# Performance work log

Hardware: AMD Instinct MI355X
Metric: run time of the kernel (lower is better)

The kernel has to match this reference:

```python
import jax, jax.numpy as jnp
import numpy as np

N, T, J, NB = 2048, 81, 16, 15
D_ATT, HEADS, SEQ, D_LIN, NOISE = 48, 6, 31, 256, 45
BN_EPS, LN_EPS, SLOPE = 1e-5, 1e-6, 0.01

# Human3.6M 16-joint skeleton bone (parent, child) pairs
_BONES = [(0,1),(1,2),(2,3),(0,4),(4,5),(5,6),(0,7),(7,8),(8,9),(9,10),(8,11),(11,12),(12,13),(8,14),(14,15)]
BONES_P = np.array([p for p, c in _BONES])
BONES_C = np.array([c for p, c in _BONES])
_parent = {c: p for p, c in _BONES}
_bone_of = {c: i for i, (p, c) in enumerate(_BONES)}
_M = np.zeros((NB, J), np.float32)  # M[i,j]=1 iff bone i lies on root->joint j chain
for j in range(1, J):
    jj = j
    while jj != 0:
        _M[_bone_of[jj], j] = 1.0
        jj = _parent[jj]
M_BONE2POSE = jnp.asarray(_M)
FIXED_MASK = jnp.ones((NB,), jnp.float32).at[jnp.array([6, 7])].set(0.0)  # torso bones kept fixed


def _layer_norm(t, a, b):
    mean = t.mean(-1, keepdims=True)
    # torch.std default is unbiased (ddof=1); module divides by (std + eps)
    std = jnp.sqrt(((t - mean) ** 2).sum(-1, keepdims=True) / (t.shape[-1] - 1))
    return a * (t - mean) / (std + LN_EPS) + b


def _leaky(x):
    return jnp.where(x >= 0, x, SLOPE * x)


def _axis_angle_to_matrix(v):
    # Rodrigues: v (..., 3) axis-angle -> (..., 3, 3)
    theta = jnp.linalg.norm(v, axis=-1, keepdims=True)
    k = v / jnp.maximum(theta, 1e-8)
    c = jnp.cos(theta)[..., None]
    s = jnp.sin(theta)[..., None]
    kx, ky, kz = k[..., 0], k[..., 1], k[..., 2]
    z = jnp.zeros_like(kx)
    K = jnp.stack([jnp.stack([z, -kz, ky], -1),
                   jnp.stack([kz, z, -kx], -1),
                   jnp.stack([-ky, kx, z], -1)], -2)
    kk = k[..., :, None] * k[..., None, :]
    return c * jnp.eye(3, dtype=v.dtype) + s * K + (1 - c) * kk


def setup_inputs() -> dict:
    key = jax.random.key(0)
    ks = jax.random.split(key, 12)
    w = lambda k, shape, scale=0.05: jax.random.normal(k, shape, jnp.float32) * scale
    return {
        'inputs_3d': jax.random.normal(ks[0], (N, 1, T, J, 3), jnp.float32),
        'noise': jax.random.normal(ks[1], (N, NOISE), jnp.float32),
        'enc_w': w(ks[2], (D_ATT, 3)), 'enc_b': jnp.zeros((D_ATT,), jnp.float32),
        'enc_bn_g': jnp.ones((D_ATT,), jnp.float32), 'enc_bn_b': jnp.zeros((D_ATT,), jnp.float32),
        'ln_a': jnp.ones((D_ATT,), jnp.float32), 'ln_b': jnp.zeros((D_ATT,), jnp.float32),
        'wq': w(ks[3], (D_ATT, D_ATT)), 'bq': jnp.zeros((D_ATT,), jnp.float32),
        'wk': w(ks[4], (D_ATT, D_ATT)), 'bk': jnp.zeros((D_ATT,), jnp.float32),
        'wv': w(ks[5], (D_ATT, D_ATT)), 'bv': jnp.zeros((D_ATT,), jnp.float32),
        'wo': w(ks[6], (D_ATT, D_ATT)), 'bo': jnp.zeros((D_ATT,), jnp.float32),
        'w1': w(ks[7], (D_LIN, SEQ * D_ATT)), 'b1': jnp.zeros((D_LIN,), jnp.float32),
        'bn1_g': jnp.ones((D_LIN,), jnp.float32), 'bn1_b': jnp.zeros((D_LIN,), jnp.float32),
        'w2': w(ks[8], (NB * 4, D_LIN)), 'b2': w(ks[9], (NB * 4,), 0.1),
    }


def reference(inputs_3d, noise, enc_w, enc_b, enc_bn_g, enc_bn_b, ln_a, ln_b,
              wq, bq, wk, bk, wv, bv, wo, bo, w1, b1, bn1_g, bn1_b, w2, b2):
    x5 = inputs_3d[:, 0]                                  # (n, T, 16, 3)
    root = x5[:, :, :1, :]
    x = x5 - root                                         # root-centered
    bvec = x[..., BONES_C, :] - x[..., BONES_P, :]        # (n, T, 15, 3)
    blen = jnp.linalg.norm(bvec, axis=-1, keepdims=True)
    bunit = bvec / blen
    n, t_len = x.shape[0], x.shape[1]
    mid = (t_len - 1) // 2

    x_ = x[:, mid].reshape(n, -1)                         # (n, 48)
    y = jnp.concatenate([x_, noise], axis=-1).reshape(n, SEQ, 3)
    # Conv1d(k=1) == per-token linear; BatchNorm eval (running mean 0, var 1); Dropout off
    y = jax.nn.relu((y @ enc_w.T + enc_b) * enc_bn_g / jnp.sqrt(1.0 + BN_EPS) + enc_bn_b)

    # tiny 6-head self-attention with pre-LayerNorm and residual
    h = _layer_norm(y, ln_a, ln_b)
    d = D_ATT // HEADS
    q = (h @ wq.T + bq).reshape(n, SEQ, HEADS, d).transpose(0, 2, 1, 3)
    k = (h @ wk.T + bk).reshape(n, SEQ, HEADS, d).transpose(0, 2, 1, 3)
    v = (h @ wv.T + bv).reshape(n, SEQ, HEADS, d).transpose(0, 2, 1, 3)
    probs = jax.nn.softmax(jnp.einsum('nhqd,nhkd->nhqk', q, k) / (d ** 0.5), axis=-1)
    ctx = jnp.einsum('nhqk,nhkd->nhqd', probs, v).transpose(0, 2, 1, 3).reshape(n, SEQ, D_ATT)
    y = y + (ctx @ wo.T + bo)

    y = y.reshape(n, -1)                                  # (n, 1488)
    y = _leaky((y @ w1.T + b1) * bn1_g / jnp.sqrt(1.0 + BN_EPS) + bn1_b)
    y = _leaky(y @ w2.T + b2).reshape(n, NB, 4)           # (n, 15, 4)

    axis = y[..., :3]
    axis = axis / jnp.linalg.norm(axis, axis=-1, keepdims=True)
    theta = y[..., 3:4] / t_len                           # (n, 15, 1)
    t_idx = jnp.arange(t_len, dtype=y.dtype)              # (T,)
    vaa = axis[:, None] * (theta[:, None] * t_idx[None, :, None, None])  # (n, T, 15, 3)
    R = _axis_angle_to_matrix(vaa)                        # (n, T, 15, 3, 3)
    mod_unit = jnp.einsum('ntbij,ntbj->ntbi', R, bunit)
    mask = FIXED_MASK[None, None, :, None]
    mod_unit = mod_unit * mask + bunit * (1 - mask)
    ba_diff = 1 - jnp.sum(mod_unit * bunit, axis=-1)      # (n, T, 15)
    mod_bone = mod_unit * blen
    out = jnp.einsum('ntbc,bj->ntjc', mod_bone, M_BONE2POSE) + root  # (n, T, 16, 3)
    return out, ba_diff
```

## Files before the change

kernel.cpp:

```cpp
#include <hip/hip_runtime.h>
#include <math.h>

#define NS   2048
#define TL   81
#define NBN  15
#define DA   48
#define SQL  31
#define KD   1488
#define DL   256
#define MID  40

#define INV_SQRT_BN 0.99999500003749969f
#define SCALE_ATT   0.35355339059327373f

__global__ __launch_bounds__(256)
void attn_kernel(const float* __restrict__ x5, const float* __restrict__ noise,
                 const float* __restrict__ enc_w, const float* __restrict__ enc_b,
                 const float* __restrict__ enc_g, const float* __restrict__ enc_bb,
                 const float* __restrict__ ln_a, const float* __restrict__ ln_b,
                 const float* __restrict__ wq, const float* __restrict__ bq,
                 const float* __restrict__ wk, const float* __restrict__ bk,
                 const float* __restrict__ wv, const float* __restrict__ bv,
                 const float* __restrict__ wo, const float* __restrict__ bo,
                 float* __restrict__ y2)
{
    __shared__ float s93[96];
    __shared__ float sy[32*49];
    __shared__ float sh[32*49];
    __shared__ float sW[3*48*49];
    __shared__ __align__(16) float sQKV[32*148];
    __shared__ float smean[32], sinv[32];

    const int tid = threadIdx.x;
    const int n = blockIdx.x;

    if (tid < 93) {
        float v;
        if (tid < 48) {
            const float* base = x5 + ((size_t)n*TL + MID)*48;
            v = base[tid] - base[tid % 3];
        } else {
            v = noise[(size_t)n*45 + (tid-48)];
        }
        s93[tid] = v;
    }
    #pragma unroll
    for (int l=0; l<9; l++){
        int idx = tid + l*256;
        int f = idx/48, c = idx - f*48;
        int o = f*49 + c;
        sW[o]        = wq[idx];
        sW[2352 + o] = wk[idx];
        sW[4704 + o] = wv[idx];
    }
    __syncthreads();

    for (int idx=tid; idx<SQL*DA; idx+=256){
        int s = idx/48, f = idx - s*48;
        float a = enc_b[f]
                + s93[s*3+0]*enc_w[f*3+0]
                + s93[s*3+1]*enc_w[f*3+1]
                + s93[s*3+2]*enc_w[f*3+2];
        float v = a * (enc_g[f]*INV_SQRT_BN) + enc_bb[f];
        sy[s*49+f] = fmaxf(v, 0.0f);
    }
    __syncthreads();

    if (tid < SQL){
        float m = 0.f;
        for (int f=0; f<48; f++) m += sy[tid*49+f];
        m *= (1.0f/48.0f);
        float vs = 0.f;
        for (int f=0; f<48; f++){ float d = sy[tid*49+f]-m; vs += d*d; }
        float sd = sqrtf(vs * (1.0f/47.0f));
        smean[tid] = m;
        sinv[tid]  = 1.0f/(sd + 1e-6f);
    }
    __syncthreads();

    for (int idx=tid; idx<SQL*DA; idx+=256){
        int s = idx/48, f = idx - s*48;
        sh[s*49+f] = ln_a[f]*(sy[s*49+f]-smean[s])*sinv[s] + ln_b[f];
    }
    __syncthreads();

    if (tid < 192){
        const int sg = tid/24, fg = tid - (tid/24)*24;
        const int arr = fg >> 3;
        const int f0  = (fg & 7)*6;
        const float* wb = sW + arr*2352 + f0*49;
        const float* hb = sh + sg*4*49;
        float a0[6]={0,0,0,0,0,0}, a1[6]={0,0,0,0,0,0};
        float a2[6]={0,0,0,0,0,0}, a3[6]={0,0,0,0,0,0};
        for (int c=0; c<48; c++){
            float h0 = hb[c], h1 = hb[49+c], h2 = hb[98+c], h3 = hb[147+c];
            #pragma unroll
            for (int i=0;i<6;i++){
                float w = wb[i*49+c];
                a0[i] += h0*w; a1[i] += h1*w; a2[i] += h2*w; a3[i] += h3*w;
            }
        }
        const float* bias = (arr==0)? bq : (arr==1? bk : bv);
        #pragma unroll
        for (int i=0;i<6;i++){
            float b = bias[f0+i];
            int col = arr*48 + f0 + i;
            sQKV[(sg*4+0)*148 + col] = a0[i] + b;
            sQKV[(sg*4+1)*148 + col] = a1[i] + b;
            sQKV[(sg*4+2)*148 + col] = a2[i] + b;
            sQKV[(sg*4+3)*148 + col] = a3[i] + b;
        }
    }
    __syncthreads();

    #pragma unroll
    for (int l=0; l<9; l++){
        int idx = tid + l*256;
        sW[(idx/48)*49 + (idx%48)] = wo[idx];
    }
    if (tid < 186){
        const int hd = tid/31, qi = tid - (tid/31)*31;
        const float4 q0 = *(const float4*)(sQKV + qi*148 + hd*8);
        const float4 q1 = *(const float4*)(sQKV + qi*148 + hd*8 + 4);
        float sc[31]; float mx = -1e30f;
        for (int ki=0; ki<31; ki++){
            const float4 k0 = *(const float4*)(sQKV + ki*148 + 48 + hd*8);
            const float4 k1 = *(const float4*)(sQKV + ki*148 + 48 + hd*8 + 4);
            float d = q0.x*k0.x + q0.y*k0.y + q0.z*k0.z + q0.w*k0.w
                    + q1.x*k1.x + q1.y*k1.y + q1.z*k1.z + q1.w*k1.w;
            d *= SCALE_ATT;
            sc[ki] = d; mx = fmaxf(mx, d);
        }
        float ssum = 0.f;
        for (int ki=0; ki<31; ki++){ float e = expf(sc[ki]-mx); sc[ki]=e; ssum += e; }
        float rin = 1.0f/ssum;
        float4 c0 = {0,0,0,0}, c1 = {0,0,0,0};
        for (int ki=0; ki<31; ki++){
            float p = sc[ki];
            const float4 v0 = *(const float4*)(sQKV + ki*148 + 96 + hd*8);
            const float4 v1 = *(const float4*)(sQKV + ki*148 + 96 + hd*8 + 4);
            c0.x += p*v0.x; c0.y += p*v0.y; c0.z += p*v0.z; c0.w += p*v0.w;
            c1.x += p*v1.x; c1.y += p*v1.y; c1.z += p*v1.z; c1.w += p*v1.w;
        }
        float* cb = sh + qi*49 + hd*8;
        cb[0]=c0.x*rin; cb[1]=c0.y*rin; cb[2]=c0.z*rin; cb[3]=c0.w*rin;
        cb[4]=c1.x*rin; cb[5]=c1.y*rin; cb[6]=c1.z*rin; cb[7]=c1.w*rin;
    }
    __syncthreads();

    if (tid < 192){
        const int sg = tid/12, fg = tid - (tid/12)*12;
        const int f0 = fg*4;
        const float* wb = sW + f0*49;
        const float* cb = sh + sg*2*49;
        float a0[4]={0,0,0,0}, a1[4]={0,0,0,0};
        for (int c=0; c<48; c++){
            float x0 = cb[c], x1 = cb[49+c];
            #pragma unroll
            for (int i=0;i<4;i++){
                float w = wb[i*49+c];
                a0[i] += x0*w; a1[i] += x1*w;
            }
        }
        {
            int s = sg*2;
            if (s < 31){
                float* dst = y2 + (size_t)n*KD + s*48 + f0;
                const float* yb = sy + s*49 + f0;
                #pragma unroll
                for (int i=0;i<4;i++) dst[i] = yb[i] + a0[i] + bo[f0+i];
            }
        }
        {
            int s = sg*2+1;
            if (s < 31){
                float* dst = y2 + (size_t)n*KD + s*48 + f0;
                const float* yb = sy + s*49 + f0;
                #pragma unroll
                for (int i=0;i<4;i++) dst[i] = yb[i] + a1[i] + bo[f0+i];
            }
        }
    }
}

#define KSP 6
#define KPS 248
#define KCH 8

__global__ __launch_bounds__(256)
void gemm1_kernel(const float* __restrict__ y2, const float* __restrict__ w1,
                  float* __restrict__ y3raw, int use_partial)
{
    __shared__ __align__(16) float sB[KCH*256];
    __shared__ __align__(16) float sA[KCH*20];
    const int tid = threadIdx.x;
    const int bx = blockIdx.x;
    const int m0 = (bx & 127) * 16;
    const int split = bx >> 7;
    const int ks0 = split * KPS;
    const int c0 = (tid & 15)*4 + (tid >> 6)*64;
    const int r0 = ((tid >> 4) & 3)*4;

    const int bn = tid >> 1;
    const int bg = (tid & 1)*4;
    const int ar = tid >> 1;
    const int ag = (tid & 1)*4;

    float acc[4][4];
    #pragma unroll
    for (int i=0;i<4;i++)
        #pragma unroll
        for (int j=0;j<4;j++) acc[i][j]=0.f;

    for (int ch=0; ch<31; ch++){
        const int k0 = ks0 + ch*KCH;
        float4 b0v = *(const float4*)(w1 + (size_t)bn*KD        + k0 + bg);
        float4 b1v = *(const float4*)(w1 + (size_t)(bn+128)*KD  + k0 + bg);
        float4 av;
        if (tid < 32) av = *(const float4*)(y2 + (size_t)(m0+ar)*KD + k0 + ag);
        __syncthreads();
        sB[(bg+0)*256 + bn] = b0v.x;  sB[(bg+1)*256 + bn] = b0v.y;
        sB[(bg+2)*256 + bn] = b0v.z;  sB[(bg+3)*256 + bn] = b0v.w;
        sB[(bg+0)*256 + bn+128] = b1v.x;  sB[(bg+1)*256 + bn+128] = b1v.y;
        sB[(bg+2)*256 + bn+128] = b1v.z;  sB[(bg+3)*256 + bn+128] = b1v.w;
        if (tid < 32){
            sA[(ag+0)*20 + ar] = av.x;  sA[(ag+1)*20 + ar] = av.y;
            sA[(ag+2)*20 + ar] = av.z;  sA[(ag+3)*20 + ar] = av.w;
        }
        __syncthreads();
        #pragma unroll
        for (int kk=0; kk<KCH; kk++){
            float4 b = *(const float4*)(sB + kk*256 + c0);
            float4 a = *(const float4*)(sA + kk*20 + r0);
            acc[0][0] += a.x*b.x; acc[0][1] += a.x*b.y; acc[0][2] += a.x*b.z; acc[0][3] += a.x*b.w;
            acc[1][0] += a.y*b.x; acc[1][1] += a.y*b.y; acc[1][2] += a.y*b.z; acc[1][3] += a.y*b.w;
            acc[2][0] += a.z*b.x; acc[2][1] += a.z*b.y; acc[2][2] += a.z*b.z; acc[2][3] += a.z*b.w;
            acc[3][0] += a.w*b.x; acc[3][1] += a.w*b.y; acc[3][2] += a.w*b.z; acc[3][3] += a.w*b.w;
        }
    }

    if (use_partial){
        float* dst = y3raw + (size_t)split*NS*DL;
        #pragma unroll
        for (int i=0;i<4;i++){
            float4 v; v.x=acc[i][0]; v.y=acc[i][1]; v.z=acc[i][2]; v.w=acc[i][3];
            *(float4*)(dst + (size_t)(m0+r0+i)*DL + c0) = v;
        }
    } else {
        #pragma unroll
        for (int i=0;i<4;i++)
            #pragma unroll
            for (int j=0;j<4;j++)
                atomicAdd(y3raw + (size_t)(m0+r0+i)*DL + c0 + j, acc[i][j]);
    }
}

__global__ __launch_bounds__(256)
void head_kernel(const float* __restrict__ y3raw, const float* __restrict__ w2,
                 const float* __restrict__ b2, const float* __restrict__ b1,
                 const float* __restrict__ g1, const float* __restrict__ bb1,
                 float* __restrict__ at, int nsl)
{
    __shared__ float swc[64*60];
    __shared__ __align__(16) float sy3[16*256];
    __shared__ float sy4[16*61];
    const int tid = threadIdx.x;
    const int n0 = blockIdx.x * 16;

    #pragma unroll
    for (int l=0;l<4;l++){
        int idx = tid + l*256;
        int s = idx >> 6, i4 = (idx & 63) << 2;
        const float* src = y3raw + (size_t)(n0+s)*256 + i4;
        float4 v = *(const float4*)(src);
        if (nsl == 6){
            #pragma unroll
            for (int sl=1; sl<6; sl++){
                float4 p = *(const float4*)(src + (size_t)sl*NS*DL);
                v.x += p.x; v.y += p.y; v.z += p.z; v.w += p.w;
            }
        }
        const float4 vb = *(const float4*)(b1 + i4);
        const float4 vg = *(const float4*)(g1 + i4);
        const float4 vs = *(const float4*)(bb1 + i4);
        v.x = (v.x + vb.x)*(vg.x*INV_SQRT_BN) + vs.x;  v.x = v.x>=0.f? v.x : 0.01f*v.x;
        v.y = (v.y + vb.y)*(vg.y*INV_SQRT_BN) + vs.y;  v.y = v.y>=0.f? v.y : 0.01f*v.y;
        v.z = (v.z + vb.z)*(vg.z*INV_SQRT_BN) + vs.z;  v.z = v.z>=0.f? v.z : 0.01f*v.z;
        v.w = (v.w + vb.w)*(vg.w*INV_SQRT_BN) + vs.w;  v.w = v.w>=0.f? v.w : 0.01f*v.w;
        *(float4*)(sy3 + s*256 + i4) = v;
    }

    float acc[4]; int ss[4], mm[4];
    #pragma unroll
    for (int l=0;l<4;l++){
        int uu = tid + l*256;
        ss[l]=0; mm[l]=0; acc[l]=0.f;
        if (uu < 960){ ss[l]=uu/60; mm[l]=uu-ss[l]*60; acc[l]=b2[mm[l]]; }
    }

    for (int ch=0; ch<4; ch++){
        const int i0 = ch*64;
        __syncthreads();
        #pragma unroll
        for (int l=0;l<15;l++){
            int idx = tid + l*256;
            int m = idx >> 6, io = idx & 63;
            swc[io*60 + m] = w2[(size_t)m*256 + i0 + io];
        }
        __syncthreads();
        #pragma unroll
        for (int l=0;l<4;l++){
            int uu = tid + l*256;
            if (uu < 960){
                const float* yy = sy3 + ss[l]*256 + i0;
                float a = acc[l];
                #pragma unroll 8
                for (int io=0; io<64; io++) a += yy[io]*swc[io*60 + mm[l]];
                acc[l] = a;
            }
        }
    }
    __syncthreads();
    #pragma unroll
    for (int l=0;l<4;l++){
        int uu = tid + l*256;
        if (uu < 960){
            float a = acc[l];
            sy4[ss[l]*61 + mm[l]] = a>=0.f? a : 0.01f*a;
        }
    }
    __syncthreads();
    if (tid < 240){
        int s = tid/15, b = tid - s*15;
        const float* y4 = sy4 + s*61 + b*4;
        float ax=y4[0], ay=y4[1], az=y4[2], th=y4[3];
        float nr = sqrtf(ax*ax+ay*ay+az*az);
        float4 o;
        o.x = ax/nr; o.y = ay/nr; o.z = az/nr; o.w = th/81.0f;
        *(float4*)(at + (size_t)(n0+s)*60 + b*4) = o;
    }
}

__global__ __launch_bounds__(256)
void pose_kernel(const float* __restrict__ x5, const float* __restrict__ at,
                 float* __restrict__ out)
{
    const int gid = blockIdx.x*256 + threadIdx.x;
    if (gid >= NS*TL) return;
    const int n = gid / TL;
    const int t = gid - n*TL;
    const float ft = (float)t;

    float4 pv[12];
    {
        const float4* src = (const float4*)(x5 + (size_t)gid*48);
        #pragma unroll
        for (int i=0;i<12;i++) pv[i] = src[i];
    }
    float* p = (float*)pv;
    const float4* ab = (const float4*)(at + (size_t)n*60);

    float4 posv[12];
    float* pos = (float*)posv;
    pos[0]=p[0]; pos[1]=p[1]; pos[2]=p[2];
    float ba[15];

    const int PJ[15] = {0,1,2,0,4,5,0,7,8,9,8,11,12,8,14};
    const int CJ[15] = {1,2,3,4,5,6,7,8,9,10,11,12,13,14,15};

    #pragma unroll
    for (int b=0;b<15;b++){
        const int pj = PJ[b], cj = CJ[b];
        float bx = p[cj*3+0]-p[pj*3+0];
        float by = p[cj*3+1]-p[pj*3+1];
        float bz = p[cj*3+2]-p[pj*3+2];
        float bl = sqrtf(bx*bx+by*by+bz*bz);
        float ux = bx/bl, uy = by/bl, uz = bz/bl;
        float mx, my, mz;
        if (b==6 || b==7){
            mx=ux; my=uy; mz=uz;
        } else {
            float4 a = ab[b];
            float ang = a.w * ft;
            float cs = cosf(ang), sn = sinf(ang);
            float kd = a.x*ux + a.y*uy + a.z*uz;
            float cx = a.y*uz - a.z*uy;
            float cy = a.z*ux - a.x*uz;
            float cz = a.x*uy - a.y*ux;
            float oc = (1.0f-cs)*kd;
            mx = ux*cs + cx*sn + a.x*oc;
            my = uy*cs + cy*sn + a.y*oc;
            mz = uz*cs + cz*sn + a.z*oc;
        }
        ba[b] = 1.0f - (mx*ux+my*uy+mz*uz);
        pos[cj*3+0] = pos[pj*3+0] + mx*bl;
        pos[cj*3+1] = pos[pj*3+1] + my*bl;
        pos[cj*3+2] = pos[pj*3+2] + mz*bl;
    }

    {
        float4* dst = (float4*)(out + (size_t)gid*48);
        #pragma unroll
        for (int i=0;i<12;i++) dst[i] = posv[i];
    }
    {
        float* bd = out + (size_t)NS*TL*48 + (size_t)gid*15;
        #pragma unroll
        for (int b=0;b<15;b++) bd[b] = ba[b];
    }
}

extern "C" void kernel_launch(void* const* d_in, const int* in_sizes, int n_in,
                              void* d_out, int out_size, void* d_ws, size_t ws_size,
                              hipStream_t stream)
{
    const float* x5    = (const float*)d_in[0];
    const float* noise = (const float*)d_in[1];
    const float* enc_w = (const float*)d_in[2];
    const float* enc_b = (const float*)d_in[3];
    const float* enc_g = (const float*)d_in[4];
    const float* enc_bb= (const float*)d_in[5];
    const float* ln_a  = (const float*)d_in[6];
    const float* ln_b  = (const float*)d_in[7];
    const float* wq = (const float*)d_in[8];
    const float* bq = (const float*)d_in[9];
    const float* wk = (const float*)d_in[10];
    const float* bk = (const float*)d_in[11];
    const float* wv = (const float*)d_in[12];
    const float* bv = (const float*)d_in[13];
    const float* wo = (const float*)d_in[14];
    const float* bo = (const float*)d_in[15];
    const float* w1 = (const float*)d_in[16];
    const float* b1 = (const float*)d_in[17];
    const float* g1 = (const float*)d_in[18];
    const float* bb1= (const float*)d_in[19];
    const float* w2 = (const float*)d_in[20];
    const float* b2 = (const float*)d_in[21];
    float* out = (float*)d_out;

    float* ws = (float*)d_ws;
    float* y2 = ws;
    float* y3 = y2 + (size_t)NS*KD;

    const size_t need_partial = ((size_t)NS*KD + 6*(size_t)NS*DL + (size_t)NS*60) * 4;
    const int use_partial = (ws_size >= need_partial) ? 1 : 0;
    const int nsl = use_partial ? 6 : 1;
    float* at = y3 + (size_t)nsl*NS*DL;

    if (!use_partial)
        hipMemsetAsync(y3, 0, (size_t)NS*DL*sizeof(float), stream);

    attn_kernel<<<NS, 256, 0, stream>>>(x5, noise, enc_w, enc_b, enc_g, enc_bb,
                                        ln_a, ln_b, wq,bq,wk,bk,wv,bv,wo,bo, y2);
    gemm1_kernel<<<128*KSP, 256, 0, stream>>>(y2, w1, y3, use_partial);
    head_kernel<<<128, 256, 0, stream>>>(y3, w2, b2, b1, g1, bb1, at, nsl);
    pose_kernel<<<(NS*TL+255)/256, 256, 0, stream>>>(x5, at, out);

    (void)in_sizes; (void)n_in; (void)out_size;
}
```

Baseline: 250.8 us.

## Restructure attention kernel shared memory, vectorize projections, and halve head-kernel tile

The attention kernel now uses a 52-float shared row stride with float4 loads for the Q/K/V/O projections. It computes LayerNorm with 8-lane shuffle reductions, which removes two barriers and the smean/sinv arrays. Weight staging shrinks to two 48x52 slots: the V and O weights are read into registers early and written into freed slots while the softmax and V projection run, which cuts LDS use and should raise occupancy. The head kernel handles 8 samples per block instead of 16, so it launches 256 blocks rather than 128 and fills more CUs. The cost is more register pressure from the sc[31] array being kept live across barriers, and a larger staged-weight share per sample in the head kernel.

```diff
diff --git a/kernel.cpp b/kernel.cpp
--- a/kernel.cpp
+++ b/kernel.cpp
@@ -12,6 +12,8 @@
 
 #define INV_SQRT_BN 0.99999500003749969f
 #define SCALE_ATT   0.35355339059327373f
+
+#define SWLD 52
 
 __global__ __launch_bounds__(256)
 void attn_kernel(const float* __restrict__ x5, const float* __restrict__ noise,
@@ -25,11 +27,10 @@
                  float* __restrict__ y2)
 {
     __shared__ float s93[96];
-    __shared__ float sy[32*49];
-    __shared__ float sh[32*49];
-    __shared__ float sW[3*48*49];
+    __shared__ __align__(16) float sy[31*SWLD];
+    __shared__ __align__(16) float sh[32*SWLD];
+    __shared__ __align__(16) float sW[2*48*SWLD];
     __shared__ __align__(16) float sQKV[32*148];
-    __shared__ float smean[32], sinv[32];
 
     const int tid = threadIdx.x;
     const int n = blockIdx.x;
@@ -48,10 +49,13 @@
     for (int l=0; l<9; l++){
         int idx = tid + l*256;
         int f = idx/48, c = idx - f*48;
-        int o = f*49 + c;
-        sW[o]        = wq[idx];
-        sW[2352 + o] = wk[idx];
-        sW[4704 + o] = wv[idx];
+        sW[f*SWLD + c] = wq[idx];
+    }
+    #pragma unroll
+    for (int l=0; l<9; l++){
+        int idx = tid + l*256;
+        int f = idx/48, c = idx - f*48;
+        sW[48*SWLD + f*SWLD + c] = wk[idx];
     }
     __syncthreads();
 
@@ -62,67 +66,92 @@
                 + s93[s*3+1]*enc_w[f*3+1]
                 + s93[s*3+2]*enc_w[f*3+2];
         float v = a * (enc_g[f]*INV_SQRT_BN) + enc_bb[f];
-        sy[s*49+f] = fmaxf(v, 0.0f);
-    }
-    __syncthreads();
-
-    if (tid < SQL){
-        float m = 0.f;
-        for (int f=0; f<48; f++) m += sy[tid*49+f];
-        m *= (1.0f/48.0f);
+        sy[s*SWLD+f] = fmaxf(v, 0.0f);
+    }
+    __syncthreads();
+
+    if (tid < 248){
+        const int r = tid >> 3;
+        const int u = tid & 7;
+        const float* row = sy + r*SWLD + u*6;
+        float v[6];
+        #pragma unroll
+        for (int j=0;j<6;j++) v[j] = row[j];
+        float sm = v[0]+v[1]+v[2]+v[3]+v[4]+v[5];
+        sm += __shfl_xor(sm, 1);
+        sm += __shfl_xor(sm, 2);
+        sm += __shfl_xor(sm, 4);
+        float m = sm * (1.0f/48.0f);
         float vs = 0.f;
-        for (int f=0; f<48; f++){ float d = sy[tid*49+f]-m; vs += d*d; }
-        float sd = sqrtf(vs * (1.0f/47.0f));
-        smean[tid] = m;
-        sinv[tid]  = 1.0f/(sd + 1e-6f);
-    }
-    __syncthreads();
-
-    for (int idx=tid; idx<SQL*DA; idx+=256){
-        int s = idx/48, f = idx - s*48;
-        sh[s*49+f] = ln_a[f]*(sy[s*49+f]-smean[s])*sinv[s] + ln_b[f];
+        #pragma unroll
+        for (int j=0;j<6;j++){ float d = v[j]-m; vs += d*d; }
+        vs += __shfl_xor(vs, 1);
+        vs += __shfl_xor(vs, 2);
+        vs += __shfl_xor(vs, 4);
+        float inv = 1.0f/(sqrtf(vs*(1.0f/47.0f)) + 1e-6f);
+        float* orow = sh + r*SWLD + u*6;
+        #pragma unroll
+        for (int j=0;j<6;j++){
+            int c = u*6+j;
+            orow[j] = ln_a[c]*(v[j]-m)*inv + ln_b[c];
+        }
     }
     __syncthreads();
 
     if (tid < 192){
-        const int sg = tid/24, fg = tid - (tid/24)*24;
-        const int arr = fg >> 3;
-        const int f0  = (fg & 7)*6;
-        const float* wb = sW + arr*2352 + f0*49;
-        const float* hb = sh + sg*4*49;
-        float a0[6]={0,0,0,0,0,0}, a1[6]={0,0,0,0,0,0};
-        float a2[6]={0,0,0,0,0,0}, a3[6]={0,0,0,0,0,0};
-        for (int c=0; c<48; c++){
-            float h0 = hb[c], h1 = hb[49+c], h2 = hb[98+c], h3 = hb[147+c];
-            #pragma unroll
-            for (int i=0;i<6;i++){
-                float w = wb[i*49+c];
-                a0[i] += h0*w; a1[i] += h1*w; a2[i] += h2*w; a3[i] += h3*w;
+        const int s4  = tid / 24;
+        const int rem = tid - s4*24;
+        const int arr = rem / 12;
+        const int f4  = rem - arr*12;
+        const int f0  = f4*4;
+        const int s0  = s4*4;
+        const float* wbase = sW + arr*48*SWLD + f0*SWLD;
+        const float* hbase = sh + s0*SWLD;
+        float acc[4][4];
+        #pragma unroll
+        for (int j=0;j<4;j++){ acc[j][0]=0.f; acc[j][1]=0.f; acc[j][2]=0.f; acc[j][3]=0.f; }
+        int c0 = f0;
+        #pragma unroll
+        for (int cc=0; cc<12; cc++){
+            float4 wr[4], hr[4];
+            #pragma unroll
+            for (int i=0;i<4;i++) wr[i] = *(const float4*)(wbase + i*SWLD + c0);
+            #pragma unroll
+            for (int j=0;j<4;j++) hr[j] = *(const float4*)(hbase + j*SWLD + c0);
+            #pragma unroll
+            for (int j=0;j<4;j++){
+                #pragma unroll
+                for (int i=0;i<4;i++){
+                    acc[j][i] += hr[j].x*wr[i].x + hr[j].y*wr[i].y
+                               + hr[j].z*wr[i].z + hr[j].w*wr[i].w;
+                }
             }
-        }
-        const float* bias = (arr==0)? bq : (arr==1? bk : bv);
-        #pragma unroll
-        for (int i=0;i<6;i++){
-            float b = bias[f0+i];
-            int col = arr*48 + f0 + i;
-            sQKV[(sg*4+0)*148 + col] = a0[i] + b;
-            sQKV[(sg*4+1)*148 + col] = a1[i] + b;
-            sQKV[(sg*4+2)*148 + col] = a2[i] + b;
-            sQKV[(sg*4+3)*148 + col] = a3[i] + b;
-        }
-    }
-    __syncthreads();
-
-    #pragma unroll
-    for (int l=0; l<9; l++){
-        int idx = tid + l*256;
-        sW[(idx/48)*49 + (idx%48)] = wo[idx];
-    }
+            c0 += 4; if (c0 == 48) c0 = 0;
+        }
+        const float* bias = arr ? bk : bq;
+        const float4 b4 = *(const float4*)(bias + f0);
+        #pragma unroll
+        for (int j=0;j<4;j++){
+            float4 o;
+            o.x = acc[j][0] + b4.x; o.y = acc[j][1] + b4.y;
+            o.z = acc[j][2] + b4.z; o.w = acc[j][3] + b4.w;
+            *(float4*)(sQKV + (s0+j)*148 + arr*48 + f0) = o;
+        }
+    }
+    __syncthreads();
+
+    float wvr[9];
+    #pragma unroll
+    for (int l=0; l<9; l++) wvr[l] = wv[tid + l*256];
+
+    float sc[31]; float rin = 0.f;
+    int hd = 0, qi = 0;
     if (tid < 186){
-        const int hd = tid/31, qi = tid - (tid/31)*31;
+        hd = tid/31; qi = tid - hd*31;
         const float4 q0 = *(const float4*)(sQKV + qi*148 + hd*8);
         const float4 q1 = *(const float4*)(sQKV + qi*148 + hd*8 + 4);
-        float sc[31]; float mx = -1e30f;
+        float mx = -1e30f;
+        #pragma unroll
         for (int ki=0; ki<31; ki++){
             const float4 k0 = *(const float4*)(sQKV + ki*148 + 48 + hd*8);
             const float4 k1 = *(const float4*)(sQKV + ki*148 + 48 + hd*8 + 4);
@@ -132,52 +161,123 @@
             sc[ki] = d; mx = fmaxf(mx, d);
         }
         float ssum = 0.f;
+        #pragma unroll
         for (int ki=0; ki<31; ki++){ float e = expf(sc[ki]-mx); sc[ki]=e; ssum += e; }
-        float rin = 1.0f/ssum;
-        float4 c0 = {0,0,0,0}, c1 = {0,0,0,0};
+        rin = 1.0f/ssum;
+    }
+    #pragma unroll
+    for (int l=0; l<9; l++){
+        int idx = tid + l*256;
+        int f = idx/48, c = idx - f*48;
+        sW[f*SWLD + c] = wvr[l];
+    }
+    __syncthreads();
+
+    float wor[9];
+    #pragma unroll
+    for (int l=0; l<9; l++) wor[l] = wo[tid + l*256];
+
+    if (tid < 192){
+        const int s2 = tid / 12;
+        const int f4 = tid - s2*12;
+        const int f0 = f4*4;
+        const float* wbase = sW + f0*SWLD;
+        const float* hbase = sh + (s2*2)*SWLD;
+        float acc[2][4];
+        #pragma unroll
+        for (int j=0;j<2;j++){ acc[j][0]=0.f; acc[j][1]=0.f; acc[j][2]=0.f; acc[j][3]=0.f; }
+        int c0 = f0;
+        #pragma unroll
+        for (int cc=0; cc<12; cc++){
+            float4 wr[4];
+            #pragma unroll
+            for (int i=0;i<4;i++) wr[i] = *(const float4*)(wbase + i*SWLD + c0);
+            const float4 h0 = *(const float4*)(hbase + c0);
+            const float4 h1 = *(const float4*)(hbase + SWLD + c0);
+            #pragma unroll
+            for (int i=0;i<4;i++){
+                acc[0][i] += h0.x*wr[i].x + h0.y*wr[i].y + h0.z*wr[i].z + h0.w*wr[i].w;
+                acc[1][i] += h1.x*wr[i].x + h1.y*wr[i].y + h1.z*wr[i].z + h1.w*wr[i].w;
+            }
+            c0 += 4; if (c0 == 48) c0 = 0;
+        }
+        const float4 b4 = *(const float4*)(bv + f0);
+        #pragma unroll
+        for (int j=0;j<2;j++){
+            float4 o;
+            o.x = acc[j][0] + b4.x; o.y = acc[j][1] + b4.y;
+            o.z = acc[j][2] + b4.z; o.w = acc[j][3] + b4.w;
+            *(float4*)(sQKV + (s2*2+j)*148 + 96 + f0) = o;
+        }
+    }
+    #pragma unroll
+    for (int l=0; l<9; l++){
+        int idx = tid + l*256;
+        int f = idx/48, c = idx - f*48;
+        sW[48*SWLD + f*SWLD + c] = wor[l];
+    }
+    __syncthreads();
+
+    if (tid < 186){
+        float4 c0v = {0,0,0,0}, c1v = {0,0,0,0};
+        #pragma unroll
         for (int ki=0; ki<31; ki++){
             float p = sc[ki];
             const float4 v0 = *(const float4*)(sQKV + ki*148 + 96 + hd*8);
             const float4 v1 = *(const float4*)(sQKV + ki*148 + 96 + hd*8 + 4);
-            c0.x += p*v0.x; c0.y += p*v0.y; c0.z += p*v0.z; c0.w += p*v0.w;
-            c1.x += p*v1.x; c1.y += p*v1.y; c1.z += p*v1.z; c1.w += p*v1.w;
-        }
-        float* cb = sh + qi*49 + hd*8;
-        cb[0]=c0.x*rin; cb[1]=c0.y*rin; cb[2]=c0.z*rin; cb[3]=c0.w*rin;
-        cb[4]=c1.x*rin; cb[5]=c1.y*rin; cb[6]=c1.z*rin; cb[7]=c1.w*rin;
+            c0v.x += p*v0.x; c0v.y += p*v0.y; c0v.z += p*v0.z; c0v.w += p*v0.w;
+            c1v.x += p*v1.x; c1v.y += p*v1.y; c1v.z += p*v1.z; c1v.w += p*v1.w;
+        }
+        float* cb = sh + qi*SWLD + hd*8;
+        float4 o0, o1;
+        o0.x = c0v.x*rin; o0.y = c0v.y*rin; o0.z = c0v.z*rin; o0.w = c0v.w*rin;
+        o1.x = c1v.x*rin; o1.y = c1v.y*rin; o1.z = c1v.z*rin; o1.w = c1v.w*rin;
+        *(float4*)(cb)     = o0;
+        *(float4*)(cb + 4) = o1;
     }
     __syncthreads();
 
     if (tid < 192){
-        const int sg = tid/12, fg = tid - (tid/12)*12;
-        const int f0 = fg*4;
-        const float* wb = sW + f0*49;
-        const float* cb = sh + sg*2*49;
-        float a0[4]={0,0,0,0}, a1[4]={0,0,0,0};
-        for (int c=0; c<48; c++){
-            float x0 = cb[c], x1 = cb[49+c];
+        const int s2 = tid / 12;
+        const int f4 = tid - s2*12;
+        const int f0 = f4*4;
+        const float* wbase = sW + 48*SWLD + f0*SWLD;
+        const float* cbase = sh + (s2*2)*SWLD;
+        float acc[2][4];
+        #pragma unroll
+        for (int j=0;j<2;j++){ acc[j][0]=0.f; acc[j][1]=0.f; acc[j][2]=0.f; acc[j][3]=0.f; }
+        int c0 = f0;
+        #pragma unroll
+        for (int cc=0; cc<12; cc++){
+            float4 wr[4];
+            #pragma unroll
+            for (int i=0;i<4;i++) wr[i] = *(const float4*)(wbase + i*SWLD + c0);
+            const float4 h0 = *(const float4*)(cbase + c0);
+            const float4 h1 = *(const float4*)(cbase + SWLD + c0);
             #pragma unroll
             for (int i=0;i<4;i++){
-                float w = wb[i*49+c];
-                a0[i] += x0*w; a1[i] += x1*w;
+                acc[0][i] += h0.x*wr[i].x + h0.y*wr[i].y + h0.z*wr[i].z + h0.w*wr[i].w;
+                acc[1][i] += h1.x*wr[i].x + h1.y*wr[i].y + h1.z*wr[i].z + h1.w*wr[i].w;
             }
-        }
+            c0 += 4; if (c0 == 48) c0 = 0;
+        }
+        const float4 b4 = *(const float4*)(bo + f0);
         {
-            int s = sg*2;
+            int s = s2*2;
+            const float4 yv = *(const float4*)(sy + s*SWLD + f0);
+            float4 o;
+            o.x = yv.x + acc[0][0] + b4.x; o.y = yv.y + acc[0][1] + b4.y;
+            o.z = yv.z + acc[0][2] + b4.z; o.w = yv.w + acc[0][3] + b4.w;
+            *(float4*)(y2 + (size_t)n*KD + s*48 + f0) = o;
+        }
+        {
+            int s = s2*2+1;
             if (s < 31){
-                float* dst = y2 + (size_t)n*KD + s*48 + f0;
-                const float* yb = sy + s*49 + f0;
-                #pragma unroll
-                for (int i=0;i<4;i++) dst[i] = yb[i] + a0[i] + bo[f0+i];
-            }
-        }
-        {
-            int s = sg*2+1;
-            if (s < 31){
-                float* dst = y2 + (size_t)n*KD + s*48 + f0;
-                const float* yb = sy + s*49 + f0;
-                #pragma unroll
-                for (int i=0;i<4;i++) dst[i] = yb[i] + a1[i] + bo[f0+i];
+                const float4 yv = *(const float4*)(sy + s*SWLD + f0);
+                float4 o;
+                o.x = yv.x + acc[1][0] + b4.x; o.y = yv.y + acc[1][1] + b4.y;
+                o.z = yv.z + acc[1][2] + b4.z; o.w = yv.w + acc[1][3] + b4.w;
+                *(float4*)(y2 + (size_t)n*KD + s*48 + f0) = o;
             }
         }
     }
@@ -262,13 +362,13 @@
                  float* __restrict__ at, int nsl)
 {
     __shared__ float swc[64*60];
-    __shared__ __align__(16) float sy3[16*256];
-    __shared__ float sy4[16*61];
+    __shared__ __align__(16) float sy3[8*256];
+    __shared__ float sy4[8*61];
     const int tid = threadIdx.x;
-    const int n0 = blockIdx.x * 16;
-
-    #pragma unroll
-    for (int l=0;l<4;l++){
+    const int n0 = blockIdx.x * 8;
+
+    #pragma unroll
+    for (int l=0;l<2;l++){
         int idx = tid + l*256;
         int s = idx >> 6, i4 = (idx & 63) << 2;
         const float* src = y3raw + (size_t)(n0+s)*256 + i4;
@@ -290,12 +390,12 @@
         *(float4*)(sy3 + s*256 + i4) = v;
     }
 
-    float acc[4]; int ss[4], mm[4];
-    #pragma unroll
-    for (int l=0;l<4;l++){
+    float acc[2]; int ss[2], mm[2];
+    #pragma unroll
+    for (int l=0;l<2;l++){
         int uu = tid + l*256;
         ss[l]=0; mm[l]=0; acc[l]=0.f;
-        if (uu < 960){ ss[l]=uu/60; mm[l]=uu-ss[l]*60; acc[l]=b2[mm[l]]; }
+        if (uu < 480){ ss[l]=uu/60; mm[l]=uu-ss[l]*60; acc[l]=b2[mm[l]]; }
     }
 
     for (int ch=0; ch<4; ch++){
@@ -309,9 +409,9 @@
         }
         __syncthreads();
         #pragma unroll
-        for (int l=0;l<4;l++){
+        for (int l=0;l<2;l++){
             int uu = tid + l*256;
-            if (uu < 960){
+            if (uu < 480){
                 const float* yy = sy3 + ss[l]*256 + i0;
                 float a = acc[l];
                 #pragma unroll 8
@@ -322,15 +422,15 @@
     }
     __syncthreads();
     #pragma unroll
-    for (int l=0;l<4;l++){
+    for (int l=0;l<2;l++){
         int uu = tid + l*256;
-        if (uu < 960){
+        if (uu < 480){
             float a = acc[l];
             sy4[ss[l]*61 + mm[l]] = a>=0.f? a : 0.01f*a;
         }
     }
     __syncthreads();
-    if (tid < 240){
+    if (tid < 120){
         int s = tid/15, b = tid - s*15;
         const float* y4 = sy4 + s*61 + b*4;
         float ax=y4[0], ay=y4[1], az=y4[2], th=y4[3];
@@ -453,7 +553,7 @@
     attn_kernel<<<NS, 256, 0, stream>>>(x5, noise, enc_w, enc_b, enc_g, enc_bb,
                                         ln_a, ln_b, wq,bq,wk,bk,wv,bv,wo,bo, y2);
     gemm1_kernel<<<128*KSP, 256, 0, stream>>>(y2, w1, y3, use_partial);
-    head_kernel<<<128, 256, 0, stream>>>(y3, w2, b2, b1, g1, bb1, at, nsl);
+    head_kernel<<<NS/8, 256, 0, stream>>>(y3, w2, b2, b1, g1, bb1, at, nsl);
     pose_kernel<<<(NS*TL+255)/256, 256, 0, stream>>>(x5, at, out);
 
     (void)in_sizes; (void)n_in; (void)out_size;
```

Result: slower. 281.5 us (+12.2%).

## Process two samples per attention block and shrink head kernel tiles

Applied to the files above, without the earlier changes.

The attention kernel now handles two samples per block. It loads the Q/K/V/O weights into shared memory once, so weight staging is amortized over both samples, and it prefetches the next sample's inputs during the layernorm phase. Layernorm statistics are now computed with 8-lane shuffle reductions in place of a single-thread serial loop. The head kernel now processes 8 samples per block instead of 16, launching more blocks for better parallelism at the cost of more redundant w2 loads. The larger shared footprint and the added launch-bounds occupancy hint may change how many attention blocks fit per CU.

```diff
diff --git a/kernel.cpp b/kernel.cpp
--- a/kernel.cpp
+++ b/kernel.cpp
@@ -9,11 +9,12 @@
 #define KD   1488
 #define DL   256
 #define MID  40
+#define SAMP 2
 
 #define INV_SQRT_BN 0.99999500003749969f
 #define SCALE_ATT   0.35355339059327373f
 
-__global__ __launch_bounds__(256)
+__global__ __launch_bounds__(256, 4)
 void attn_kernel(const float* __restrict__ x5, const float* __restrict__ noise,
                  const float* __restrict__ enc_w, const float* __restrict__ enc_b,
                  const float* __restrict__ enc_g, const float* __restrict__ enc_bb,
@@ -27,20 +28,19 @@
     __shared__ float s93[96];
     __shared__ float sy[32*49];
     __shared__ float sh[32*49];
-    __shared__ float sW[3*48*49];
+    __shared__ float sW[4*48*49];
     __shared__ __align__(16) float sQKV[32*148];
-    __shared__ float smean[32], sinv[32];
 
     const int tid = threadIdx.x;
-    const int n = blockIdx.x;
+    const int n0 = blockIdx.x * SAMP;
 
     if (tid < 93) {
         float v;
         if (tid < 48) {
-            const float* base = x5 + ((size_t)n*TL + MID)*48;
+            const float* base = x5 + ((size_t)n0*TL + MID)*48;
             v = base[tid] - base[tid % 3];
         } else {
-            v = noise[(size_t)n*45 + (tid-48)];
+            v = noise[(size_t)n0*45 + (tid-48)];
         }
         s93[tid] = v;
     }
@@ -52,132 +52,153 @@
         sW[o]        = wq[idx];
         sW[2352 + o] = wk[idx];
         sW[4704 + o] = wv[idx];
+        sW[7056 + o] = wo[idx];
     }
     __syncthreads();
 
-    for (int idx=tid; idx<SQL*DA; idx+=256){
-        int s = idx/48, f = idx - s*48;
-        float a = enc_b[f]
-                + s93[s*3+0]*enc_w[f*3+0]
-                + s93[s*3+1]*enc_w[f*3+1]
-                + s93[s*3+2]*enc_w[f*3+2];
-        float v = a * (enc_g[f]*INV_SQRT_BN) + enc_bb[f];
-        sy[s*49+f] = fmaxf(v, 0.0f);
-    }
-    __syncthreads();
-
-    if (tid < SQL){
-        float m = 0.f;
-        for (int f=0; f<48; f++) m += sy[tid*49+f];
-        m *= (1.0f/48.0f);
-        float vs = 0.f;
-        for (int f=0; f<48; f++){ float d = sy[tid*49+f]-m; vs += d*d; }
-        float sd = sqrtf(vs * (1.0f/47.0f));
-        smean[tid] = m;
-        sinv[tid]  = 1.0f/(sd + 1e-6f);
-    }
-    __syncthreads();
-
-    for (int idx=tid; idx<SQL*DA; idx+=256){
-        int s = idx/48, f = idx - s*48;
-        sh[s*49+f] = ln_a[f]*(sy[s*49+f]-smean[s])*sinv[s] + ln_b[f];
-    }
-    __syncthreads();
-
-    if (tid < 192){
-        const int sg = tid/24, fg = tid - (tid/24)*24;
-        const int arr = fg >> 3;
-        const int f0  = (fg & 7)*6;
-        const float* wb = sW + arr*2352 + f0*49;
-        const float* hb = sh + sg*4*49;
-        float a0[6]={0,0,0,0,0,0}, a1[6]={0,0,0,0,0,0};
-        float a2[6]={0,0,0,0,0,0}, a3[6]={0,0,0,0,0,0};
-        for (int c=0; c<48; c++){
-            float h0 = hb[c], h1 = hb[49+c], h2 = hb[98+c], h3 = hb[147+c];
+    for (int si=0; si<SAMP; si++){
+        const int n = n0 + si;
+        if (si) __syncthreads();
+
+        for (int idx=tid; idx<SQL*DA; idx+=256){
+            int s = idx/48, f = idx - s*48;
+            float a = enc_b[f]
+                    + s93[s*3+0]*enc_w[f*3+0]
+                    + s93[s*3+1]*enc_w[f*3+1]
+                    + s93[s*3+2]*enc_w[f*3+2];
+            float v = a * (enc_g[f]*INV_SQRT_BN) + enc_bb[f];
+            sy[s*49+f] = fmaxf(v, 0.0f);
+        }
+        __syncthreads();
+
+        if (tid < 248){
+            const int r = tid >> 3;
+            const int u = tid & 7;
+            const float* row = sy + r*49 + u*6;
+            float v[6];
+            #pragma unroll
+            for (int j=0;j<6;j++) v[j] = row[j];
+            float sm = v[0]+v[1]+v[2]+v[3]+v[4]+v[5];
+            sm += __shfl_xor(sm, 1);
+            sm += __shfl_xor(sm, 2);
+            sm += __shfl_xor(sm, 4);
+            float m = sm * (1.0f/48.0f);
+            float vs = 0.f;
+            #pragma unroll
+            for (int j=0;j<6;j++){ float d = v[j]-m; vs += d*d; }
+            vs += __shfl_xor(vs, 1);
+            vs += __shfl_xor(vs, 2);
+            vs += __shfl_xor(vs, 4);
+            float inv = 1.0f/(sqrtf(vs*(1.0f/47.0f)) + 1e-6f);
+            float* orow = sh + r*49 + u*6;
+            #pragma unroll
+            for (int j=0;j<6;j++){
+                int c = u*6+j;
+                orow[j] = ln_a[c]*(v[j]-m)*inv + ln_b[c];
+            }
+        }
+        if (si+1 < SAMP && tid < 93){
+            float v;
+            if (tid < 48) {
+                const float* base = x5 + ((size_t)(n+1)*TL + MID)*48;
+                v = base[tid] - base[tid % 3];
+            } else {
+                v = noise[(size_t)(n+1)*45 + (tid-48)];
+            }
+            s93[tid] = v;
+        }
+        __syncthreads();
+
+        if (tid < 192){
+            const int sg = tid/24, fg = tid - (tid/24)*24;
+            const int arr = fg >> 3;
+            const int f0  = (fg & 7)*6;
+            const float* wb = sW + arr*2352 + f0*49;
+            const float* hb = sh + sg*4*49;
+            float a0[6]={0,0,0,0,0,0}, a1[6]={0,0,0,0,0,0};
+            float a2[6]={0,0,0,0,0,0}, a3[6]={0,0,0,0,0,0};
+            for (int c=0; c<48; c++){
+                float h0 = hb[c], h1 = hb[49+c], h2 = hb[98+c], h3 = hb[147+c];
+                #pragma unroll
+                for (int i=0;i<6;i++){
+                    float w = wb[i*49+c];
+                    a0[i] += h0*w; a1[i] += h1*w; a2[i] += h2*w; a3[i] += h3*w;
+                }
+            }
+            const float* bias = (arr==0)? bq : (arr==1? bk : bv);
             #pragma unroll
             for (int i=0;i<6;i++){
-                float w = wb[i*49+c];
-                a0[i] += h0*w; a1[i] += h1*w; a2[i] += h2*w; a3[i] += h3*w;
-            }
-        }
-        const float* bias = (arr==0)? bq : (arr==1? bk : bv);
-        #pragma unroll
-        for (int i=0;i<6;i++){
-            float b = bias[f0+i];
-            int col = arr*48 + f0 + i;
-            sQKV[(sg*4+0)*148 + col] = a0[i] + b;
-            sQKV[(sg*4+1)*148 + col] = a1[i] + b;
-            sQKV[(sg*4+2)*148 + col] = a2[i] + b;
-            sQKV[(sg*4+3)*148 + col] = a3[i] + b;
-        }
-    }
-    __syncthreads();
-
-    #pragma unroll
-    for (int l=0; l<9; l++){
-        int idx = tid + l*256;
-        sW[(idx/48)*49 + (idx%48)] = wo[idx];
-    }
-    if (tid < 186){
-        const int hd = tid/31, qi = tid - (tid/31)*31;
-        const float4 q0 = *(const float4*)(sQKV + qi*148 + hd*8);
-        const float4 q1 = *(const float4*)(sQKV + qi*148 + hd*8 + 4);
-        float sc[31]; float mx = -1e30f;
-        for (int ki=0; ki<31; ki++){
-            const float4 k0 = *(const float4*)(sQKV + ki*148 + 48 + hd*8);
-            const float4 k1 = *(const float4*)(sQKV + ki*148 + 48 + hd*8 + 4);
-            float d = q0.x*k0.x + q0.y*k0.y + q0.z*k0.z + q0.w*k0.w
-                    + q1.x*k1.x + q1.y*k1.y + q1.z*k1.z + q1.w*k1.w;
-            d *= SCALE_ATT;
-            sc[ki] = d; mx = fmaxf(mx, d);
-        }
-        float ssum = 0.f;
-        for (int ki=0; ki<31; ki++){ float e = expf(sc[ki]-mx); sc[ki]=e; ssum += e; }
-        float rin = 1.0f/ssum;
-        float4 c0 = {0,0,0,0}, c1 = {0,0,0,0};
-        for (int ki=0; ki<31; ki++){
-            float p = sc[ki];
-            const float4 v0 = *(const float4*)(sQKV + ki*148 + 96 + hd*8);
-            const float4 v1 = *(const float4*)(sQKV + ki*148 + 96 + hd*8 + 4);
-            c0.x += p*v0.x; c0.y += p*v0.y; c0.z += p*v0.z; c0.w += p*v0.w;
-            c1.x += p*v1.x; c1.y += p*v1.y; c1.z += p*v1.z; c1.w += p*v1.w;
-        }
-        float* cb = sh + qi*49 + hd*8;
-        cb[0]=c0.x*rin; cb[1]=c0.y*rin; cb[2]=c0.z*rin; cb[3]=c0.w*rin;
-        cb[4]=c1.x*rin; cb[5]=c1.y*rin; cb[6]=c1.z*rin; cb[7]=c1.w*rin;
-    }
-    __syncthreads();
-
-    if (tid < 192){
-        const int sg = tid/12, fg = tid - (tid/12)*12;
-        const int f0 = fg*4;
-        const float* wb = sW + f0*49;
-        const float* cb = sh + sg*2*49;
-        float a0[4]={0,0,0,0}, a1[4]={0,0,0,0};
-        for (int c=0; c<48; c++){
-            float x0 = cb[c], x1 = cb[49+c];
-            #pragma unroll
-            for (int i=0;i<4;i++){
-                float w = wb[i*49+c];
-                a0[i] += x0*w; a1[i] += x1*w;
-            }
-        }
-        {
-            int s = sg*2;
-            if (s < 31){
-                float* dst = y2 + (size_t)n*KD + s*48 + f0;
-                const float* yb = sy + s*49 + f0;
+                float b = bias[f0+i];
+                int col = arr*48 + f0 + i;
+                sQKV[(sg*4+0)*148 + col] = a0[i] + b;
+                sQKV[(sg*4+1)*148 + col] = a1[i] + b;
+                sQKV[(sg*4+2)*148 + col] = a2[i] + b;
+                sQKV[(sg*4+3)*148 + col] = a3[i] + b;
+            }
+        }
+        __syncthreads();
+
+        if (tid < 186){
+            const int hd = tid/31, qi = tid - (tid/31)*31;
+            const float4 q0 = *(const float4*)(sQKV + qi*148 + hd*8);
+            const float4 q1 = *(const float4*)(sQKV + qi*148 + hd*8 + 4);
+            float sc[31]; float mx = -1e30f;
+            for (int ki=0; ki<31; ki++){
+                const float4 k0 = *(const float4*)(sQKV + ki*148 + 48 + hd*8);
+                const float4 k1 = *(const float4*)(sQKV + ki*148 + 48 + hd*8 + 4);
+                float d = q0.x*k0.x + q0.y*k0.y + q0.z*k0.z + q0.w*k0.w
+                        + q1.x*k1.x + q1.y*k1.y + q1.z*k1.z + q1.w*k1.w;
+                d *= SCALE_ATT;
+                sc[ki] = d; mx = fmaxf(mx, d);
+            }
+            float ssum = 0.f;
+            for (int ki=0; ki<31; ki++){ float e = expf(sc[ki]-mx); sc[ki]=e; ssum += e; }
+            float rin = 1.0f/ssum;
+            float4 c0 = {0,0,0,0}, c1 = {0,0,0,0};
+            for (int ki=0; ki<31; ki++){
+                float p = sc[ki];
+                const float4 v0 = *(const float4*)(sQKV + ki*148 + 96 + hd*8);
+                const float4 v1 = *(const float4*)(sQKV + ki*148 + 96 + hd*8 + 4);
+                c0.x += p*v0.x; c0.y += p*v0.y; c0.z += p*v0.z; c0.w += p*v0.w;
+                c1.x += p*v1.x; c1.y += p*v1.y; c1.z += p*v1.z; c1.w += p*v1.w;
+            }
+            float* cb = sh + qi*49 + hd*8;
+            cb[0]=c0.x*rin; cb[1]=c0.y*rin; cb[2]=c0.z*rin; cb[3]=c0.w*rin;
+            cb[4]=c1.x*rin; cb[5]=c1.y*rin; cb[6]=c1.z*rin; cb[7]=c1.w*rin;
+        }
+        __syncthreads();
+
+        if (tid < 192){
+            const int sg = tid/12, fg = tid - (tid/12)*12;
+            const int f0 = fg*4;
+            const float* wb = sW + 7056 + f0*49;
+            const float* cb = sh + sg*2*49;
+            float a0[4]={0,0,0,0}, a1[4]={0,0,0,0};
+            for (int c=0; c<48; c++){
+                float x0 = cb[c], x1 = cb[49+c];
                 #pragma unroll
-                for (int i=0;i<4;i++) dst[i] = yb[i] + a0[i] + bo[f0+i];
-            }
-        }
-        {
-            int s = sg*2+1;
-            if (s < 31){
-                float* dst = y2 + (size_t)n*KD + s*48 + f0;
-                const float* yb = sy + s*49 + f0;
-                #pragma unroll
-                for (int i=0;i<4;i++) dst[i] = yb[i] + a1[i] + bo[f0+i];
+                for (int i=0;i<4;i++){
+                    float w = wb[i*49+c];
+                    a0[i] += x0*w; a1[i] += x1*w;
+                }
+            }
+            {
+                int s = sg*2;
+                if (s < 31){
+                    float* dst = y2 + (size_t)n*KD + s*48 + f0;
+                    const float* yb = sy + s*49 + f0;
+                    #pragma unroll
+                    for (int i=0;i<4;i++) dst[i] = yb[i] + a0[i] + bo[f0+i];
+                }
+            }
+            {
+                int s = sg*2+1;
+                if (s < 31){
+                    float* dst = y2 + (size_t)n*KD + s*48 + f0;
+                    const float* yb = sy + s*49 + f0;
+                    #pragma unroll
+                    for (int i=0;i<4;i++) dst[i] = yb[i] + a1[i] + bo[f0+i];
+                }
             }
         }
     }
@@ -262,13 +283,13 @@
                  float* __restrict__ at, int nsl)
 {
     __shared__ float swc[64*60];
-    __shared__ __align__(16) float sy3[16*256];
-    __shared__ float sy4[16*61];
+    __shared__ __align__(16) float sy3[8*256];
+    __shared__ float sy4[8*61];
     const int tid = threadIdx.x;
-    const int n0 = blockIdx.x * 16;
-
-    #pragma unroll
-    for (int l=0;l<4;l++){
+    const int n0 = blockIdx.x * 8;
+
+    #pragma unroll
+    for (int l=0;l<2;l++){
         int idx = tid + l*256;
         int s = idx >> 6, i4 = (idx & 63) << 2;
         const float* src = y3raw + (size_t)(n0+s)*256 + i4;
@@ -290,12 +311,12 @@
         *(float4*)(sy3 + s*256 + i4) = v;
     }
 
-    float acc[4]; int ss[4], mm[4];
-    #pragma unroll
-    for (int l=0;l<4;l++){
+    float acc[2]; int ss[2], mm[2];
+    #pragma unroll
+    for (int l=0;l<2;l++){
         int uu = tid + l*256;
         ss[l]=0; mm[l]=0; acc[l]=0.f;
-        if (uu < 960){ ss[l]=uu/60; mm[l]=uu-ss[l]*60; acc[l]=b2[mm[l]]; }
+        if (uu < 480){ ss[l]=uu/60; mm[l]=uu-ss[l]*60; acc[l]=b2[mm[l]]; }
     }
 
     for (int ch=0; ch<4; ch++){
@@ -309,9 +330,9 @@
         }
         __syncthreads();
         #pragma unroll
-        for (int l=0;l<4;l++){
+        for (int l=0;l<2;l++){
             int uu = tid + l*256;
-            if (uu < 960){
+            if (uu < 480){
                 const float* yy = sy3 + ss[l]*256 + i0;
                 float a = acc[l];
                 #pragma unroll 8
@@ -322,15 +343,15 @@
     }
     __syncthreads();
     #pragma unroll
-    for (int l=0;l<4;l++){
+    for (int l=0;l<2;l++){
         int uu = tid + l*256;
-        if (uu < 960){
+        if (uu < 480){
             float a = acc[l];
             sy4[ss[l]*61 + mm[l]] = a>=0.f? a : 0.01f*a;
         }
     }
     __syncthreads();
-    if (tid < 240){
+    if (tid < 120){
         int s = tid/15, b = tid - s*15;
         const float* y4 = sy4 + s*61 + b*4;
         float ax=y4[0], ay=y4[1], az=y4[2], th=y4[3];
@@ -450,10 +471,10 @@
     if (!use_partial)
         hipMemsetAsync(y3, 0, (size_t)NS*DL*sizeof(float), stream);
 
-    attn_kernel<<<NS, 256, 0, stream>>>(x5, noise, enc_w, enc_b, enc_g, enc_bb,
-                                        ln_a, ln_b, wq,bq,wk,bk,wv,bv,wo,bo, y2);
+    attn_kernel<<<NS/SAMP, 256, 0, stream>>>(x5, noise, enc_w, enc_b, enc_g, enc_bb,
+                                             ln_a, ln_b, wq,bq,wk,bk,wv,bv,wo,bo, y2);
     gemm1_kernel<<<128*KSP, 256, 0, stream>>>(y2, w1, y3, use_partial);
-    head_kernel<<<128, 256, 0, stream>>>(y3, w2, b2, b1, g1, bb1, at, nsl);
+    head_kernel<<<NS/8, 256, 0, stream>>>(y3, w2, b2, b1, g1, bb1, at, nsl);
     pose_kernel<<<(NS*TL+255)/256, 256, 0, stream>>>(x5, at, out);
 
     (void)in_sizes; (void)n_in; (void)out_size;
```

Result: slower. 268.9 us (+7.2%).
